# Performance work log

Hardware: AMD Instinct MI355X
Metric: run time of the kernel (lower is better)

Reference implementation:

```python
import jax, jax.numpy as jnp
import numpy as np

N = 50000      # nodes
E = 1600000    # edges per graph
IN = 64
HID = 64
OUT = 64


def _gat_conv(x, edge_index, W, a_src, a_dst, bias):
    """PyG GATConv, heads=1, add_self_loops=True, negative_slope=0.2."""
    n = x.shape[0]
    h = x @ W                                   # [N, d]
    loop = jnp.arange(n, dtype=edge_index.dtype)
    src = jnp.concatenate([edge_index[0], loop])
    dst = jnp.concatenate([edge_index[1], loop])
    e = jax.nn.leaky_relu((h @ a_src)[src] + (h @ a_dst)[dst], negative_slope=0.2)
    m = jax.ops.segment_max(e, dst, num_segments=n)          # stable edge-softmax per dst
    w = jnp.exp(e - m[dst])
    denom = jax.ops.segment_sum(w, dst, num_segments=n)
    alpha = w / denom[dst]                                   # [E+N]
    out = jax.ops.segment_sum(h[src] * alpha[:, None], dst, num_segments=n)
    return out + bias


def setup_inputs() -> dict:
    key = jax.random.key(0)
    ks = jax.random.split(key, 32)

    def glorot(k, shape):
        fan_out = shape[1] if len(shape) > 1 else 1
        lim = (6.0 / (shape[0] + fan_out)) ** 0.5
        return jax.random.uniform(k, shape, minval=-lim, maxval=lim, dtype=jnp.float32)

    inp = {
        "x_ind": jax.random.normal(ks[0], (N, IN), jnp.float32),
        "x_pos": jax.random.normal(ks[1], (N, IN), jnp.float32),
        "edge_ind": jax.random.randint(ks[2], (2, E), 0, N, dtype=jnp.int32),
        "edge_pos": jax.random.randint(ks[3], (2, E), 0, N, dtype=jnp.int32),
        "w1_ind": glorot(ks[4], (IN, HID)),
        "as1_ind": glorot(ks[5], (HID,)),
        "ad1_ind": glorot(ks[6], (HID,)),
        "b1_ind": jnp.zeros((HID,), jnp.float32),
        "w2_ind": glorot(ks[7], (HID, OUT)),
        "as2_ind": glorot(ks[8], (OUT,)),
        "ad2_ind": glorot(ks[9], (OUT,)),
        "b2_ind": jnp.zeros((OUT,), jnp.float32),
        "w1_pos": glorot(ks[10], (IN, HID)),
        "as1_pos": glorot(ks[11], (HID,)),
        "ad1_pos": glorot(ks[12], (HID,)),
        "b1_pos": jnp.zeros((HID,), jnp.float32),
        "w2_pos": glorot(ks[13], (HID, OUT)),
        "as2_pos": glorot(ks[14], (OUT,)),
        "ad2_pos": glorot(ks[15], (OUT,)),
        "b2_pos": jnp.zeros((OUT,), jnp.float32),
        "first_hop_att": glorot(ks[16], (2, HID)),
        "att_weight": glorot(ks[17], (2, OUT)),
        "mlp_w": glorot(ks[18], (OUT, 1)),
        "mlp_b": jnp.zeros((1,), jnp.float32),
    }
    return inp


def reference(x_ind, x_pos, edge_ind, edge_pos,
              w1_ind, as1_ind, ad1_ind, b1_ind,
              w2_ind, as2_ind, ad2_ind, b2_ind,
              w1_pos, as1_pos, ad1_pos, b1_pos,
              w2_pos, as2_pos, ad2_pos, b2_pos,
              first_hop_att, att_weight, mlp_w, mlp_b):
    h_i = jax.nn.relu(_gat_conv(x_ind, edge_ind, w1_ind, as1_ind, ad1_ind, b1_ind))
    h_p = jax.nn.relu(_gat_conv(x_pos, edge_pos, w1_pos, as1_pos, ad1_pos, b1_pos))
    # first-hop branch attention over the two graphs
    s1 = jnp.stack([jnp.sum(first_hop_att[0] * h_i, axis=1),
                    jnp.sum(first_hop_att[1] * h_p, axis=1)], axis=0)  # [2, N]
    a1 = jax.nn.softmax(s1, axis=0)
    fused = a1[0][:, None] * h_i + a1[1][:, None] * h_p
    g_i = _gat_conv(fused, edge_ind, w2_ind, as2_ind, ad2_ind, b2_ind)
    g_p = _gat_conv(fused, edge_pos, w2_pos, as2_pos, ad2_pos, b2_pos)
    s2 = jnp.stack([jnp.sum(att_weight[0] * g_i, axis=1),
                    jnp.sum(att_weight[1] * g_p, axis=1)], axis=0)
    a2 = jax.nn.softmax(s2, axis=0)
    x = a2[0][:, None] * g_i + a2[1][:, None] * g_p
    return x @ mlp_w + mlp_b                    # [N, 1]
```

## Files before the change

### kernel.cpp

```cpp
#include <hip/hip_runtime.h>
#include <hip/hip_fp16.h>

#define ND 64
#define BG 128
#define MAXB 1024
#define PCH 16384
#define CAP 4608

__device__ __forceinline__ float lrelu(float x) { return x > 0.f ? x : 0.2f * x; }

__device__ __forceinline__ float wave_sum(float v) {
#pragma unroll
    for (int m = 32; m > 0; m >>= 1) v += __shfl_xor(v, m, 64);
    return v;
}

__device__ __forceinline__ void fma8(float* acc, float w, int4 raw) {
    union { int4 i; __half h[8]; } u;
    u.i = raw;
#pragma unroll
    for (int i = 0; i < 8; i++) acc[i] = fmaf(w, __half2float(u.h[i]), acc[i]);
}


__global__ void init_cursor(int* __restrict__ bcursor, int nb) {
    int t = threadIdx.x;
    if (t < nb) bcursor[t] = t * CAP;
}

__device__ void partition_body(int* hist, int* lcur,
                               const int* __restrict__ eI, const int* __restrict__ eP,
                               int* __restrict__ bcursor, int* __restrict__ part,
                               int N, int E, int nb) {
    int t = threadIdx.x;
    int total = 2 * E;
    int chunkBase = blockIdx.x * PCH;
    int cnt = min(PCH, total - chunkBase);
    if (t < nb) hist[t] = 0;
    __syncthreads();

    if (cnt == PCH) {
        int pk[16];
        unsigned bkp[8];
#pragma unroll
        for (int it = 0; it < 4; it++) {
            int i = t * 4 + it * 4096;
            int e = chunkBase + i;
            int sv[4], dv[4];
            if (e + 3 < E) {
                int4 a = *(const int4*)(eI + e);
                int4 b = *(const int4*)(eI + E + e);
                sv[0] = a.x; sv[1] = a.y; sv[2] = a.z; sv[3] = a.w;
                dv[0] = b.x; dv[1] = b.y; dv[2] = b.z; dv[3] = b.w;
            } else if (e >= E) {
                int4 a = *(const int4*)(eP + (e - E));
                int4 b = *(const int4*)(eP + E + (e - E));
                sv[0] = a.x; sv[1] = a.y; sv[2] = a.z; sv[3] = a.w;
                dv[0] = b.x + N; dv[1] = b.y + N; dv[2] = b.z + N; dv[3] = b.w + N;
            } else {
#pragma unroll
                for (int k = 0; k < 4; k++) {
                    int ee = e + k;
                    if (ee < E) { sv[k] = eI[ee]; dv[k] = eI[E + ee]; }
                    else        { sv[k] = eP[ee - E]; dv[k] = N + eP[E + ee - E]; }
                }
            }
#pragma unroll
            for (int k = 0; k < 4; k++) {
                int j = it * 4 + k;
                int bk = dv[k] >> 7;
                pk[j] = (sv[k] << 8) | (dv[k] & 255);
                atomicAdd(&hist[bk], 1);
                if ((j & 1) == 0) bkp[j >> 1] = (unsigned)bk;
                else bkp[j >> 1] |= (unsigned)bk << 16;
            }
        }
        __syncthreads();
        if (t < nb) lcur[t] = hist[t] ? atomicAdd(&bcursor[t], hist[t]) : 0;
        __syncthreads();
#pragma unroll
        for (int j = 0; j < 16; j++) {
            int bk = (bkp[j >> 1] >> ((j & 1) * 16)) & 0xffff;
            int pos = atomicAdd(&lcur[bk], 1);
            part[pos] = pk[j];
        }
        return;
    }

    int cnt4 = cnt & ~3;
    for (int i = t * 4; i < cnt4; i += 4096) {
        int e = chunkBase + i;
        int4 d; int base;
        if (e + 3 < E)   { d = *(const int4*)(eI + E + e); base = 0; }
        else if (e >= E) { d = *(const int4*)(eP + E + (e - E)); base = N; }
        else {
            int tmp[4];
#pragma unroll
            for (int k = 0; k < 4; k++) {
                int ee = e + k;
                tmp[k] = (ee < E) ? eI[E + ee] : N + eP[E + ee - E];
            }
            d = make_int4(tmp[0], tmp[1], tmp[2], tmp[3]); base = 0;
        }
        atomicAdd(&hist[(base + d.x) >> 7], 1);
        atomicAdd(&hist[(base + d.y) >> 7], 1);
        atomicAdd(&hist[(base + d.z) >> 7], 1);
        atomicAdd(&hist[(base + d.w) >> 7], 1);
    }
    for (int i = cnt4 + t; i < cnt; i += 1024) {
        int e = chunkBase + i;
        int idx = (e < E) ? eI[E + e] : N + eP[E + (e - E)];
        atomicAdd(&hist[idx >> 7], 1);
    }
    __syncthreads();
    if (t < nb) lcur[t] = hist[t] ? atomicAdd(&bcursor[t], hist[t]) : 0;
    __syncthreads();
    for (int i = t; i < cnt; i += 1024) {
        int e = chunkBase + i;
        int s, idx;
        if (e < E) { s = eI[e]; idx = eI[E + e]; }
        else       { s = eP[e - E]; idx = N + eP[E + (e - E)]; }
        int pos = atomicAdd(&lcur[idx >> 7], 1);
        part[pos] = (s << 8) | (idx & 255);
    }
}

__device__ void gemm_body(float* xsAll, int gb,
                          const float* __restrict__ xA, const float* __restrict__ xB,
                          const float* __restrict__ WA, const float* __restrict__ WB,
                          const float* __restrict__ asA, const float* __restrict__ adA,
                          const float* __restrict__ asB, const float* __restrict__ adB,
                          __half* __restrict__ h16, float* __restrict__ ssrc,
                          float* __restrict__ sdst, int N) {
    int half = gb & 1;
    int blk = gb >> 1;
    int wave = threadIdx.x >> 6;
    int lane = threadIdx.x & 63;
    const float* x  = half ? xB : xA;
    const float* W  = half ? WB : WA;
    const float* av_ = half ? asB : asA;
    const float* dv_ = half ? adB : adA;
    int nodeBase = (blk * 16 + wave) * 4;
    float* xs = xsAll + wave * (4 * ND);

    if (nodeBase + 3 < N) {
        *(float4*)&xs[lane * 4] = *(const float4*)&x[(size_t)nodeBase * ND + lane * 4];
    } else if (nodeBase < N) {
#pragma unroll
        for (int i = 0; i < 4; i++) {
            int gi = nodeBase * ND + lane * 4 + i;
            xs[lane * 4 + i] = (gi < N * ND) ? x[gi] : 0.f;
        }
    }
    __syncthreads();
    if (nodeBase >= N) return;

    float4 acc = {0.f, 0.f, 0.f, 0.f};
#pragma unroll
    for (int k = 0; k < ND; k++) {
        float wv = W[k * ND + lane];
        acc.x = fmaf(xs[0 * ND + k], wv, acc.x);
        acc.y = fmaf(xs[1 * ND + k], wv, acc.y);
        acc.z = fmaf(xs[2 * ND + k], wv, acc.z);
        acc.w = fmaf(xs[3 * ND + k], wv, acc.w);
    }
    float av = av_[lane], dv = dv_[lane];
    float s1x = wave_sum(acc.x * av), s2x = wave_sum(acc.x * dv);
    float s1y = wave_sum(acc.y * av), s2y = wave_sum(acc.y * dv);
    float s1z = wave_sum(acc.z * av), s2z = wave_sum(acc.z * dv);
    float s1w = wave_sum(acc.w * av), s2w = wave_sum(acc.w * dv);

    int g0 = half * N + nodeBase;
    h16[(size_t)(g0 + 0) * ND + lane] = __float2half(acc.x);
    if (nodeBase + 1 < N) h16[(size_t)(g0 + 1) * ND + lane] = __float2half(acc.y);
    if (nodeBase + 2 < N) h16[(size_t)(g0 + 2) * ND + lane] = __float2half(acc.z);
    if (nodeBase + 3 < N) h16[(size_t)(g0 + 3) * ND + lane] = __float2half(acc.w);
    if (lane == 0) {
        ssrc[g0] = s1x; sdst[g0] = s2x;
        if (nodeBase + 1 < N) { ssrc[g0 + 1] = s1y; sdst[g0 + 1] = s2y; }
        if (nodeBase + 2 < N) { ssrc[g0 + 2] = s1z; sdst[g0 + 2] = s2z; }
        if (nodeBase + 3 < N) { ssrc[g0 + 3] = s1w; sdst[g0 + 3] = s2w; }
    }
}

__global__ void __launch_bounds__(1024) part_gemm(
        const int* __restrict__ eI, const int* __restrict__ eP,
        int* __restrict__ bcursor, int* __restrict__ part,
        const float* __restrict__ xA, const float* __restrict__ xB,
        const float* __restrict__ WA, const float* __restrict__ WB,
        const float* __restrict__ asA, const float* __restrict__ adA,
        const float* __restrict__ asB, const float* __restrict__ adB,
        __half* __restrict__ h16, float* __restrict__ ssrc, float* __restrict__ sdst,
        int N, int E, int nb, int partBlocks) {
    __shared__ int smem[16 * 4 * ND];
    if (blockIdx.x < partBlocks) {
        partition_body(smem, smem + MAXB, eI, eP, bcursor, part, N, E, nb);
    } else {
        gemm_body((float*)smem, blockIdx.x - partBlocks,
                  xA, xB, WA, WB, asA, adA, asB, adB, h16, ssrc, sdst, N);
    }
}

__global__ void bucket_build(const int* __restrict__ part, const int* __restrict__ bcursor,
                             int* __restrict__ row, int* __restrict__ deg,
                             int* __restrict__ csr, int n2, int N) {
    __shared__ int lhist[BG * 8];
    __shared__ int lrow[BG * 8];
    __shared__ int slab[CAP];
    int b = blockIdx.x, t = threadIdx.x;
    int start = b * CAP;
    int cnt = min(bcursor[b] - start, CAP);
    int cnt4 = cnt & ~3;
    int t1 = (N * 1) >> 3, t2 = (N * 2) >> 3, t3 = (N * 3) >> 3, t4 = (N * 4) >> 3;
    int t5 = (N * 5) >> 3, t6 = (N * 6) >> 3, t7 = (N * 7) >> 3;
    auto key = [&](int p) {
        int s = p >> 8;
        int o = (s >= t1) + (s >= t2) + (s >= t3) + (s >= t4)
              + (s >= t5) + (s >= t6) + (s >= t7);
        return ((p & 127) << 3) | o;
    };
    lhist[t] = 0;
    __syncthreads();
    for (int j = t * 4; j < cnt4; j += 4096) {
        int4 p = *(const int4*)(part + start + j);
        atomicAdd(&lhist[key(p.x)], 1);
        atomicAdd(&lhist[key(p.y)], 1);
        atomicAdd(&lhist[key(p.z)], 1);
        atomicAdd(&lhist[key(p.w)], 1);
    }
    for (int j = cnt4 + t; j < cnt; j += 1024) atomicAdd(&lhist[key(part[start + j])], 1);
    __syncthreads();
    int v = lhist[t];
    lrow[t] = v;
    __syncthreads();
    for (int off = 1; off < 1024; off <<= 1) {
        int a = (t >= off) ? lrow[t - off] : 0;
        __syncthreads();
        lrow[t] += a;
        __syncthreads();
    }
    if (t < BG) {
        int g = b * BG + t;
        if (g < n2) {
            row[g] = start + lrow[8 * t] - lhist[8 * t];
            int d = 0;
#pragma unroll
            for (int i = 0; i < 8; i++) d += lhist[8 * t + i];
            deg[g] = d;
        }
    }
    __syncthreads();
    lhist[t] = lrow[t] - v;
    __syncthreads();
    for (int j = t * 4; j < cnt4; j += 4096) {
        int4 p = *(const int4*)(part + start + j);
        int pos;
        pos = atomicAdd(&lhist[key(p.x)], 1); slab[pos] = p.x >> 8;
        pos = atomicAdd(&lhist[key(p.y)], 1); slab[pos] = p.y >> 8;
        pos = atomicAdd(&lhist[key(p.z)], 1); slab[pos] = p.z >> 8;
        pos = atomicAdd(&lhist[key(p.w)], 1); slab[pos] = p.w >> 8;
    }
    for (int j = cnt4 + t; j < cnt; j += 1024) {
        int p = part[start + j];
        int pos = atomicAdd(&lhist[key(p)], 1);
        slab[pos] = p >> 8;
    }
    __syncthreads();
    {
        int ge = lrow[t], gs = ge - v;
        for (int i = gs + 1; i < ge; i++) {
            int x = slab[i], j2 = i - 1;
            while (j2 >= gs && slab[j2] > x) { slab[j2 + 1] = slab[j2]; j2--; }
            slab[j2 + 1] = x;
        }
    }
    __syncthreads();
    for (int j = t; j < cnt; j += 1024) csr[start + j] = slab[j];
}


__device__ __forceinline__ void gather_body(
        const int* __restrict__ csr, int start, int cnt, float sd,
        const float* __restrict__ ss, const __half* __restrict__ hh,
        int l16, int slot, int fl8, int waveBase,
        float* acc, float& denomp) {
    int c16 = min(16, cnt);
    int sj = (l16 < c16) ? csr[start + l16] : 0;
    float wj = (l16 < c16) ? __expf(lrelu(ss[sj] + sd)) : 0.f;

    for (int base = 0; base < cnt; base += 16) {
        int nb2 = base + 16;
        int sjn = 0; float svn = 0.f; int c16n = cnt - nb2;
        if (nb2 < cnt) {
            sjn = (l16 < c16n) ? csr[start + nb2 + l16] : 0;
            svn = (l16 < c16n) ? ss[sjn] : 0.f;
        }
        denomp += wj;
        int nq = (min(16, cnt - base) + 1) >> 1;
        float w0 = __shfl(wj, waveBase + slot, 64);
        int s0 = __shfl(sj, waveBase + slot, 64);
        int4 r0 = *(const int4*)(hh + (size_t)s0 * ND + fl8);
        if (nq > 1) {
            float w1 = __shfl(wj, waveBase + 2 + slot, 64);
            int s1 = __shfl(sj, waveBase + 2 + slot, 64);
            int4 r1 = *(const int4*)(hh + (size_t)s1 * ND + fl8);
            for (int c = 2; c < nq; c++) {
                float w2 = __shfl(wj, waveBase + c * 2 + slot, 64);
                int s2 = __shfl(sj, waveBase + c * 2 + slot, 64);
                int4 r2 = *(const int4*)(hh + (size_t)s2 * ND + fl8);
                fma8(acc, w0, r0);
                w0 = w1; r0 = r1;
                w1 = w2; r1 = r2;
            }
            fma8(acc, w0, r0);
            fma8(acc, w1, r1);
        } else {
            fma8(acc, w0, r0);
        }
        if (nb2 < cnt) {
            wj = (l16 < c16n) ? __expf(lrelu(svn + sd)) : 0.f;
            sj = sjn;
        }
    }
}

__global__ void agg1_att(
        const int* __restrict__ csr, const int* __restrict__ row,
        const int* __restrict__ deg, const float* __restrict__ ss1,
        const float* __restrict__ sd1, const __half* __restrict__ h16a,
        const float* __restrict__ b1A, const float* __restrict__ b1B,
        const float* __restrict__ fha,
        float* __restrict__ hfused, int N) {
    __shared__ float lds_h[2][8][ND];
    int wave = threadIdx.x >> 6, lane = threadIdx.x & 63;
    int half = wave >> 1;
    int sub = lane >> 4, l16 = lane & 15, slot = l16 >> 3, fl8 = (l16 & 7) * 8;
    int nodeIdx = (wave & 1) * 4 + sub;
    int node = blockIdx.x * 8 + nodeIdx;
    bool valid = node < N;
    int g = half * N + node;
    const float* bias = half ? b1B : b1A;
    const float* ss = ss1 + (size_t)half * N;
    const __half* hh = h16a + (size_t)half * N * ND;

    int start = valid ? row[g] : 0;
    int cnt   = valid ? deg[g] : 0;
    float sd  = valid ? sd1[g] : 0.f;
    float wself = valid ? __expf(lrelu(ss[node] + sd)) : 0.f;

    float acc[8] = {0.f, 0.f, 0.f, 0.f, 0.f, 0.f, 0.f, 0.f};
    float denomp = 0.f;
    gather_body(csr, start, cnt, sd, ss, hh, l16, slot, fl8, sub << 4, acc, denomp);

#pragma unroll
    for (int i = 0; i < 8; i++) acc[i] += __shfl_xor(acc[i], 8, 64);
#pragma unroll
    for (int m = 1; m <= 8; m <<= 1) denomp += __shfl_xor(denomp, m, 64);
    float denom = denomp + wself;

    if (slot == 0) {
        if (valid) {
            int4 rawS = *(const int4*)(hh + (size_t)node * ND + fl8);
            union { int4 i; __half h[8]; } us;
            us.i = rawS;
#pragma unroll
            for (int i = 0; i < 8; i++)
                lds_h[half][nodeIdx][fl8 + i] =
                    fmaxf((acc[i] + wself * __half2float(us.h[i])) / denom + bias[fl8 + i], 0.f);
        } else {
#pragma unroll
            for (int i = 0; i < 8; i++) lds_h[half][nodeIdx][fl8 + i] = 0.f;
        }
    }
    __syncthreads();

#pragma unroll
    for (int r = 0; r < 2; r++) {
        int n = wave * 2 + r;
        int gn = blockIdx.x * 8 + n;
        float vi = lds_h[0][n][lane], vp = lds_h[1][n][lane];
        float p0 = wave_sum(fha[lane] * vi);
        float p1 = wave_sum(fha[ND + lane] * vp);
        float mx = fmaxf(p0, p1);
        float e0 = __expf(p0 - mx), e1 = __expf(p1 - mx);
        float inv = 1.f / (e0 + e1);
        if (gn < N) hfused[(size_t)gn * ND + lane] = (e0 * vi + e1 * vp) * inv;
    }
}

__global__ void __launch_bounds__(512) gemm2_plain(
        const float* __restrict__ hfused,
        const float* __restrict__ W2A, const float* __restrict__ W2B,
        const float* __restrict__ as2A, const float* __restrict__ ad2A,
        const float* __restrict__ as2B, const float* __restrict__ ad2B,
        __half* __restrict__ h16b, float* __restrict__ ssrc2,
        float* __restrict__ sdst2, int N) {
    __shared__ float xs[16][ND];
    int t = threadIdx.x;
    int n0 = blockIdx.x * 16;
    if (t < 256) {
        int r = t >> 4, c = (t & 15) * 4;
        int n = n0 + r;
        float4 v = (n < N) ? *(const float4*)&hfused[(size_t)n * ND + c]
                           : make_float4(0.f, 0.f, 0.f, 0.f);
        *(float4*)&xs[r][c] = v;
    }
    __syncthreads();
    int wave = t >> 6, lane = t & 63;
    int half = wave >> 2;
    int nb0 = (wave & 3) * 4;
    const float* W  = half ? W2B : W2A;
    const float* av_ = half ? as2B : as2A;
    const float* dv_ = half ? ad2B : ad2A;

    float4 acc = {0.f, 0.f, 0.f, 0.f};
#pragma unroll
    for (int k = 0; k < ND; k++) {
        float wv = W[k * ND + lane];
        acc.x = fmaf(xs[nb0 + 0][k], wv, acc.x);
        acc.y = fmaf(xs[nb0 + 1][k], wv, acc.y);
        acc.z = fmaf(xs[nb0 + 2][k], wv, acc.z);
        acc.w = fmaf(xs[nb0 + 3][k], wv, acc.w);
    }
    float av = av_[lane], dv = dv_[lane];
    float s1x = wave_sum(acc.x * av), s2x = wave_sum(acc.x * dv);
    float s1y = wave_sum(acc.y * av), s2y = wave_sum(acc.y * dv);
    float s1z = wave_sum(acc.z * av), s2z = wave_sum(acc.z * dv);
    float s1w = wave_sum(acc.w * av), s2w = wave_sum(acc.w * dv);

    int node = n0 + nb0;
    int g0 = half * N + node;
    if (node + 0 < N) h16b[(size_t)(g0 + 0) * ND + lane] = __float2half(acc.x);
    if (node + 1 < N) h16b[(size_t)(g0 + 1) * ND + lane] = __float2half(acc.y);
    if (node + 2 < N) h16b[(size_t)(g0 + 2) * ND + lane] = __float2half(acc.z);
    if (node + 3 < N) h16b[(size_t)(g0 + 3) * ND + lane] = __float2half(acc.w);
    if (lane == 0) {
        if (node + 0 < N) { ssrc2[g0 + 0] = s1x; sdst2[g0 + 0] = s2x; }
        if (node + 1 < N) { ssrc2[g0 + 1] = s1y; sdst2[g0 + 1] = s2y; }
        if (node + 2 < N) { ssrc2[g0 + 2] = s1z; sdst2[g0 + 2] = s2z; }
        if (node + 3 < N) { ssrc2[g0 + 3] = s1w; sdst2[g0 + 3] = s2w; }
    }
}

__global__ void agg2_mlp(
        const int* __restrict__ csr, const int* __restrict__ row,
        const int* __restrict__ deg, const float* __restrict__ ss2,
        const float* __restrict__ sd2, const __half* __restrict__ h16b,
        const float* __restrict__ b2A, const float* __restrict__ b2B,
        const float* __restrict__ attw, const float* __restrict__ mlpw,
        const float* __restrict__ mlpb,
        float* __restrict__ out, int N) {
    __shared__ float lds_h[2][8][ND];
    int wave = threadIdx.x >> 6, lane = threadIdx.x & 63;
    int half = wave >> 1;
    int sub = lane >> 4, l16 = lane & 15, slot = l16 >> 3, fl8 = (l16 & 7) * 8;
    int nodeIdx = (wave & 1) * 4 + sub;
    int node = blockIdx.x * 8 + nodeIdx;
    bool valid = node < N;
    int g = half * N + node;
    const float* bias = half ? b2B : b2A;
    const float* ss = ss2 + (size_t)half * N;
    const __half* hh = h16b + (size_t)half * N * ND;

    int start = valid ? row[g] : 0;
    int cnt   = valid ? deg[g] : 0;
    float sd  = valid ? sd2[g] : 0.f;
    float wself = valid ? __expf(lrelu(ss[node] + sd)) : 0.f;

    float acc[8] = {0.f, 0.f, 0.f, 0.f, 0.f, 0.f, 0.f, 0.f};
    float denomp = 0.f;
    gather_body(csr, start, cnt, sd, ss, hh, l16, slot, fl8, sub << 4, acc, denomp);

#pragma unroll
    for (int i = 0; i < 8; i++) acc[i] += __shfl_xor(acc[i], 8, 64);
#pragma unroll
    for (int m = 1; m <= 8; m <<= 1) denomp += __shfl_xor(denomp, m, 64);
    float denom = denomp + wself;

    if (slot == 0) {
        if (valid) {
            int4 rawS = *(const int4*)(hh + (size_t)node * ND + fl8);
            union { int4 i; __half h[8]; } us;
            us.i = rawS;
#pragma unroll
            for (int i = 0; i < 8; i++)
                lds_h[half][nodeIdx][fl8 + i] =
                    (acc[i] + wself * __half2float(us.h[i])) / denom + bias[fl8 + i];
        } else {
#pragma unroll
            for (int i = 0; i < 8; i++) lds_h[half][nodeIdx][fl8 + i] = 0.f;
        }
    }
    __syncthreads();

#pragma unroll
    for (int r = 0; r < 2; r++) {
        int n = wave * 2 + r;
        int gn = blockIdx.x * 8 + n;
        float vi = lds_h[0][n][lane], vp = lds_h[1][n][lane];
        float s0 = wave_sum(attw[lane] * vi);
        float s1 = wave_sum(attw[ND + lane] * vp);
        float m = fmaxf(s0, s1);
        float a0 = __expf(s0 - m), a1 = __expf(s1 - m);
        float xj = (a0 * vi + a1 * vp) / (a0 + a1);
        float o = wave_sum(xj * mlpw[lane]);
        if (lane == 0 && gn < N) out[gn] = o + mlpb[0];
    }
}

extern "C" void kernel_launch(void* const* d_in, const int* in_sizes, int n_in,
                              void* d_out, int out_size, void* d_ws, size_t ws_size,
                              hipStream_t stream) {
    const int N = in_sizes[0] / ND;
    const int E = in_sizes[2] / 2;

    const float* x_ind = (const float*)d_in[0];
    const float* x_pos = (const float*)d_in[1];
    const int*   e_ind = (const int*)d_in[2];
    const int*   e_pos = (const int*)d_in[3];
    const float* w1i = (const float*)d_in[4];
    const float* as1i = (const float*)d_in[5];
    const float* ad1i = (const float*)d_in[6];
    const float* b1i = (const float*)d_in[7];
    const float* w2i = (const float*)d_in[8];
    const float* as2i = (const float*)d_in[9];
    const float* ad2i = (const float*)d_in[10];
    const float* b2i = (const float*)d_in[11];
    const float* w1p = (const float*)d_in[12];
    const float* as1p = (const float*)d_in[13];
    const float* ad1p = (const float*)d_in[14];
    const float* b1p = (const float*)d_in[15];
    const float* w2p = (const float*)d_in[16];
    const float* as2p = (const float*)d_in[17];
    const float* ad2p = (const float*)d_in[18];
    const float* b2p = (const float*)d_in[19];
    const float* fha = (const float*)d_in[20];
    const float* attw = (const float*)d_in[21];
    const float* mlpw = (const float*)d_in[22];
    const float* mlpb = (const float*)d_in[23];

    char* ws = (char*)d_ws;
    size_t off = 0;
    auto alloc = [&](size_t elems) { void* p = ws + off; off += elems * 4; return p; };

    const int n2 = 2 * N;
    const int nb = (n2 + BG - 1) / BG;

    __half* h16a = (__half*)alloc((size_t)n2 * ND / 2);
    float* ssrc1 = (float*)alloc(n2);
    float* sdst1 = (float*)alloc(n2);
    float* ssrc2 = (float*)alloc(n2);
    float* sdst2 = (float*)alloc(n2);
    int* deg    = (int*)alloc(n2);
    int* rowi   = (int*)alloc(n2);
    int* csr    = (int*)alloc((size_t)nb * CAP);
    int* bcursor= (int*)alloc(MAXB);
    int* part   = (int*)alloc((size_t)nb * CAP);
    float* hfused = (float*)alloc((size_t)N * ND);
    __half* h16b = (__half*)part;

    const int partBlocks  = (2 * E + PCH - 1) / PCH;
    const int gemm1Blocks = 2 * ((N + 63) / 64);
    const int fusedBlocks = (N + 7) / 8;
    const int gemm2Blocks = (N + 15) / 16;

    init_cursor<<<1, 1024, 0, stream>>>(bcursor, nb);
    part_gemm<<<partBlocks + gemm1Blocks, 1024, 0, stream>>>(
        e_ind, e_pos, bcursor, part,
        x_ind, x_pos, w1i, w1p, as1i, ad1i, as1p, ad1p,
        h16a, ssrc1, sdst1, N, E, nb, partBlocks);
    bucket_build<<<nb, 1024, 0, stream>>>(part, bcursor, rowi, deg, csr, n2, N);

    agg1_att<<<fusedBlocks, 256, 0, stream>>>(
        csr, rowi, deg, ssrc1, sdst1, h16a, b1i, b1p, fha, hfused, N);

    gemm2_plain<<<gemm2Blocks, 512, 0, stream>>>(
        hfused, w2i, w2p, as2i, ad2i, as2p, ad2p, h16b, ssrc2, sdst2, N);

    agg2_mlp<<<fusedBlocks, 256, 0, stream>>>(
        csr, rowi, deg, ssrc2, sdst2, h16b, b2i, b2p,
        attw, mlpw, mlpb, (float*)d_out, N);
}
```

Measured before the change: 351.0 us.

## Split aggregation per graph and defer branch attention to later kernels

The aggregation kernels no longer pair both graphs in one block with an LDS exchange and barrier. Each block now handles a single graph. Layer 1 writes fp16 per-graph outputs and attention logits, and the two-branch softmax moves into the GEMM2 load stage. Layer 2 emits only the attention and MLP dot products per graph, and a small final kernel combines them, relying on linearity of the MLP. This removes the cross-graph sync and the fp32 fused buffer, and gives each block coherent per-graph memory locality, at the cost of an extra launch and an fp16 rounding of the layer-1 output.

```diff
diff --git a/kernel.cpp b/kernel.cpp
--- a/kernel.cpp
+++ b/kernel.cpp
@@ -324,24 +324,26 @@
     }
 }
 
-__global__ void agg1_att(
-        const int* __restrict__ csr, const int* __restrict__ row,
-        const int* __restrict__ deg, const float* __restrict__ ss1,
-        const float* __restrict__ sd1, const __half* __restrict__ h16a,
-        const float* __restrict__ b1A, const float* __restrict__ b1B,
-        const float* __restrict__ fha,
-        float* __restrict__ hfused, int N) {
-    __shared__ float lds_h[2][8][ND];
-    int wave = threadIdx.x >> 6, lane = threadIdx.x & 63;
-    int half = wave >> 1;
-    int sub = lane >> 4, l16 = lane & 15, slot = l16 >> 3, fl8 = (l16 & 7) * 8;
-    int nodeIdx = (wave & 1) * 4 + sub;
-    int node = blockIdx.x * 8 + nodeIdx;
+__global__ void agg1_h(const int* __restrict__ csr, const int* __restrict__ row,
+                       const int* __restrict__ deg, const float* __restrict__ ss1,
+                       const float* __restrict__ sd1, const __half* __restrict__ h16a,
+                       const float* __restrict__ bA, const float* __restrict__ bB,
+                       const float* __restrict__ fha,
+                       __half* __restrict__ h1, float* __restrict__ plog, int N) {
+    int half = blockIdx.x & 1;
+    int wave = threadIdx.x >> 6;
+    int lane = threadIdx.x & 63;
+    int sub  = lane >> 4;
+    int l16  = lane & 15;
+    int slot = l16 >> 3;
+    int fl8  = (l16 & 7) * 8;
+    int node = ((blockIdx.x >> 1) * 4 + wave) * 4 + sub;
     bool valid = node < N;
     int g = half * N + node;
-    const float* bias = half ? b1B : b1A;
+    const float* bias = half ? bB : bA;
     const float* ss = ss1 + (size_t)half * N;
     const __half* hh = h16a + (size_t)half * N * ND;
+    const float* fhah = fha + half * ND;
 
     int start = valid ? row[g] : 0;
     int cnt   = valid ? deg[g] : 0;
@@ -358,38 +360,29 @@
     for (int m = 1; m <= 8; m <<= 1) denomp += __shfl_xor(denomp, m, 64);
     float denom = denomp + wself;
 
-    if (slot == 0) {
-        if (valid) {
-            int4 rawS = *(const int4*)(hh + (size_t)node * ND + fl8);
-            union { int4 i; __half h[8]; } us;
-            us.i = rawS;
-#pragma unroll
-            for (int i = 0; i < 8; i++)
-                lds_h[half][nodeIdx][fl8 + i] =
-                    fmaxf((acc[i] + wself * __half2float(us.h[i])) / denom + bias[fl8 + i], 0.f);
-        } else {
-#pragma unroll
-            for (int i = 0; i < 8; i++) lds_h[half][nodeIdx][fl8 + i] = 0.f;
-        }
-    }
-    __syncthreads();
-
-#pragma unroll
-    for (int r = 0; r < 2; r++) {
-        int n = wave * 2 + r;
-        int gn = blockIdx.x * 8 + n;
-        float vi = lds_h[0][n][lane], vp = lds_h[1][n][lane];
-        float p0 = wave_sum(fha[lane] * vi);
-        float p1 = wave_sum(fha[ND + lane] * vp);
-        float mx = fmaxf(p0, p1);
-        float e0 = __expf(p0 - mx), e1 = __expf(p1 - mx);
-        float inv = 1.f / (e0 + e1);
-        if (gn < N) hfused[(size_t)gn * ND + lane] = (e0 * vi + e1 * vp) * inv;
-    }
-}
-
-__global__ void __launch_bounds__(512) gemm2_plain(
-        const float* __restrict__ hfused,
+    if (!valid || slot != 0) return;
+    int4 rawS = *(const int4*)(hh + (size_t)node * ND + fl8);
+    union { int4 i; __half h[8]; } us;
+    us.i = rawS;
+    float v[8];
+#pragma unroll
+    for (int i = 0; i < 8; i++)
+        v[i] = fmaxf((acc[i] + wself * __half2float(us.h[i])) / denom + bias[fl8 + i], 0.f);
+    union { int4 i; __half h[8]; } uo;
+#pragma unroll
+    for (int i = 0; i < 8; i++) uo.h[i] = __float2half(v[i]);
+    *(int4*)&h1[(size_t)g * ND + fl8] = uo.i;
+    float p = 0.f;
+#pragma unroll
+    for (int i = 0; i < 8; i++) p = fmaf(fhah[fl8 + i], v[i], p);
+    p += __shfl_xor(p, 1, 64);
+    p += __shfl_xor(p, 2, 64);
+    p += __shfl_xor(p, 4, 64);
+    if (l16 == 0) plog[g] = p;
+}
+
+__global__ void __launch_bounds__(512) gemm2_combine(
+        const __half* __restrict__ h1, const float* __restrict__ plog,
         const float* __restrict__ W2A, const float* __restrict__ W2B,
         const float* __restrict__ as2A, const float* __restrict__ ad2A,
         const float* __restrict__ as2B, const float* __restrict__ ad2B,
@@ -401,9 +394,22 @@
     if (t < 256) {
         int r = t >> 4, c = (t & 15) * 4;
         int n = n0 + r;
-        float4 v = (n < N) ? *(const float4*)&hfused[(size_t)n * ND + c]
-                           : make_float4(0.f, 0.f, 0.f, 0.f);
-        *(float4*)&xs[r][c] = v;
+        float4 f = make_float4(0.f, 0.f, 0.f, 0.f);
+        if (n < N) {
+            union { int2 i; __half h[4]; } uI, uP;
+            uI.i = *(const int2*)&h1[(size_t)n * ND + c];
+            uP.i = *(const int2*)&h1[((size_t)N + n) * ND + c];
+            float p0 = plog[n], p1 = plog[N + n];
+            float mx = fmaxf(p0, p1);
+            float e0 = __expf(p0 - mx), e1 = __expf(p1 - mx);
+            float inv = 1.f / (e0 + e1);
+            e0 *= inv; e1 *= inv;
+            f.x = e0 * __half2float(uI.h[0]) + e1 * __half2float(uP.h[0]);
+            f.y = e0 * __half2float(uI.h[1]) + e1 * __half2float(uP.h[1]);
+            f.z = e0 * __half2float(uI.h[2]) + e1 * __half2float(uP.h[2]);
+            f.w = e0 * __half2float(uI.h[3]) + e1 * __half2float(uP.h[3]);
+        }
+        *(float4*)&xs[r][c] = f;
     }
     __syncthreads();
     int wave = t >> 6, lane = t & 63;
@@ -442,25 +448,26 @@
     }
 }
 
-__global__ void agg2_mlp(
-        const int* __restrict__ csr, const int* __restrict__ row,
-        const int* __restrict__ deg, const float* __restrict__ ss2,
-        const float* __restrict__ sd2, const __half* __restrict__ h16b,
-        const float* __restrict__ b2A, const float* __restrict__ b2B,
-        const float* __restrict__ attw, const float* __restrict__ mlpw,
-        const float* __restrict__ mlpb,
-        float* __restrict__ out, int N) {
-    __shared__ float lds_h[2][8][ND];
-    int wave = threadIdx.x >> 6, lane = threadIdx.x & 63;
-    int half = wave >> 1;
-    int sub = lane >> 4, l16 = lane & 15, slot = l16 >> 3, fl8 = (l16 & 7) * 8;
-    int nodeIdx = (wave & 1) * 4 + sub;
-    int node = blockIdx.x * 8 + nodeIdx;
+__global__ void agg2_dots(const int* __restrict__ csr, const int* __restrict__ row,
+                          const int* __restrict__ deg, const float* __restrict__ ss2,
+                          const float* __restrict__ sd2, const __half* __restrict__ h16b,
+                          const float* __restrict__ bA, const float* __restrict__ bB,
+                          const float* __restrict__ attw, const float* __restrict__ mlpw,
+                          float* __restrict__ satt, float* __restrict__ mmlp, int N) {
+    int half = blockIdx.x & 1;
+    int wave = threadIdx.x >> 6;
+    int lane = threadIdx.x & 63;
+    int sub  = lane >> 4;
+    int l16  = lane & 15;
+    int slot = l16 >> 3;
+    int fl8  = (l16 & 7) * 8;
+    int node = ((blockIdx.x >> 1) * 4 + wave) * 4 + sub;
     bool valid = node < N;
     int g = half * N + node;
-    const float* bias = half ? b2B : b2A;
+    const float* bias = half ? bB : bA;
     const float* ss = ss2 + (size_t)half * N;
     const __half* hh = h16b + (size_t)half * N * ND;
+    const float* attwh = attw + half * ND;
 
     int start = valid ? row[g] : 0;
     int cnt   = valid ? deg[g] : 0;
@@ -477,35 +484,31 @@
     for (int m = 1; m <= 8; m <<= 1) denomp += __shfl_xor(denomp, m, 64);
     float denom = denomp + wself;
 
-    if (slot == 0) {
-        if (valid) {
-            int4 rawS = *(const int4*)(hh + (size_t)node * ND + fl8);
-            union { int4 i; __half h[8]; } us;
-            us.i = rawS;
-#pragma unroll
-            for (int i = 0; i < 8; i++)
-                lds_h[half][nodeIdx][fl8 + i] =
-                    (acc[i] + wself * __half2float(us.h[i])) / denom + bias[fl8 + i];
-        } else {
-#pragma unroll
-            for (int i = 0; i < 8; i++) lds_h[half][nodeIdx][fl8 + i] = 0.f;
-        }
-    }
-    __syncthreads();
-
-#pragma unroll
-    for (int r = 0; r < 2; r++) {
-        int n = wave * 2 + r;
-        int gn = blockIdx.x * 8 + n;
-        float vi = lds_h[0][n][lane], vp = lds_h[1][n][lane];
-        float s0 = wave_sum(attw[lane] * vi);
-        float s1 = wave_sum(attw[ND + lane] * vp);
-        float m = fmaxf(s0, s1);
-        float a0 = __expf(s0 - m), a1 = __expf(s1 - m);
-        float xj = (a0 * vi + a1 * vp) / (a0 + a1);
-        float o = wave_sum(xj * mlpw[lane]);
-        if (lane == 0 && gn < N) out[gn] = o + mlpb[0];
-    }
+    if (!valid || slot != 0) return;
+    int4 rawS = *(const int4*)(hh + (size_t)node * ND + fl8);
+    union { int4 i; __half h[8]; } us;
+    us.i = rawS;
+    float pa = 0.f, pm = 0.f;
+#pragma unroll
+    for (int i = 0; i < 8; i++) {
+        float vi = (acc[i] + wself * __half2float(us.h[i])) / denom + bias[fl8 + i];
+        pa = fmaf(attwh[fl8 + i], vi, pa);
+        pm = fmaf(mlpw[fl8 + i], vi, pm);
+    }
+    pa += __shfl_xor(pa, 1, 64); pm += __shfl_xor(pm, 1, 64);
+    pa += __shfl_xor(pa, 2, 64); pm += __shfl_xor(pm, 2, 64);
+    pa += __shfl_xor(pa, 4, 64); pm += __shfl_xor(pm, 4, 64);
+    if (l16 == 0) { satt[g] = pa; mmlp[g] = pm; }
+}
+
+__global__ void final_combine(const float* __restrict__ satt, const float* __restrict__ mmlp,
+                              const float* __restrict__ mlpb, float* __restrict__ out, int N) {
+    int i = blockIdx.x * blockDim.x + threadIdx.x;
+    if (i >= N) return;
+    float s0 = satt[i], s1 = satt[N + i];
+    float m = fmaxf(s0, s1);
+    float e0 = __expf(s0 - m), e1 = __expf(s1 - m);
+    out[i] = (e0 * mmlp[i] + e1 * mmlp[N + i]) / (e0 + e1) + mlpb[0];
 }
 
 extern "C" void kernel_launch(void* const* d_in, const int* in_sizes, int n_in,
@@ -551,18 +554,22 @@
     float* sdst1 = (float*)alloc(n2);
     float* ssrc2 = (float*)alloc(n2);
     float* sdst2 = (float*)alloc(n2);
+    float* plog  = (float*)alloc(n2);
+    float* satt  = (float*)alloc(n2);
+    float* mmlp  = (float*)alloc(n2);
     int* deg    = (int*)alloc(n2);
     int* rowi   = (int*)alloc(n2);
     int* csr    = (int*)alloc((size_t)nb * CAP);
     int* bcursor= (int*)alloc(MAXB);
     int* part   = (int*)alloc((size_t)nb * CAP);
-    float* hfused = (float*)alloc((size_t)N * ND);
-    __half* h16b = (__half*)part;
+    __half* h1 = (__half*)part;
+    __half* h16b = h16a;
 
     const int partBlocks  = (2 * E + PCH - 1) / PCH;
     const int gemm1Blocks = 2 * ((N + 63) / 64);
-    const int fusedBlocks = (N + 7) / 8;
+    const int aggBlocks   = 2 * ((N + 15) / 16);
     const int gemm2Blocks = (N + 15) / 16;
+    const int finBlocks   = (N + 255) / 256;
 
     init_cursor<<<1, 1024, 0, stream>>>(bcursor, nb);
     part_gemm<<<partBlocks + gemm1Blocks, 1024, 0, stream>>>(
@@ -571,13 +578,14 @@
         h16a, ssrc1, sdst1, N, E, nb, partBlocks);
     bucket_build<<<nb, 1024, 0, stream>>>(part, bcursor, rowi, deg, csr, n2, N);
 
-    agg1_att<<<fusedBlocks, 256, 0, stream>>>(
-        csr, rowi, deg, ssrc1, sdst1, h16a, b1i, b1p, fha, hfused, N);
-
-    gemm2_plain<<<gemm2Blocks, 512, 0, stream>>>(
-        hfused, w2i, w2p, as2i, ad2i, as2p, ad2p, h16b, ssrc2, sdst2, N);
-
-    agg2_mlp<<<fusedBlocks, 256, 0, stream>>>(
-        csr, rowi, deg, ssrc2, sdst2, h16b, b2i, b2p,
-        attw, mlpw, mlpb, (float*)d_out, N);
-}
+    agg1_h<<<aggBlocks, 256, 0, stream>>>(
+        csr, rowi, deg, ssrc1, sdst1, h16a, b1i, b1p, fha, h1, plog, N);
+
+    gemm2_combine<<<gemm2Blocks, 512, 0, stream>>>(
+        h1, plog, w2i, w2p, as2i, ad2i, as2p, ad2p, h16b, ssrc2, sdst2, N);
+
+    agg2_dots<<<aggBlocks, 256, 0, stream>>>(
+        csr, rowi, deg, ssrc2, sdst2, h16b, b2i, b2p, attw, mlpw, satt, mmlp, N);
+
+    final_combine<<<finBlocks, 256, 0, stream>>>(satt, mmlp, mlpb, (float*)d_out, N);
+}
```

New measurement: 325.9 us. 1.08x faster.
